# Optimization experiments

Measured on AMD Instinct MI355X. Metric: run time of the kernel, lower is better.

The kernel has to match this reference:

```python
import jax, jax.numpy as jnp
import numpy as np

BATCH = 8192
IN_FEATURES = 4096
OUT_FEATURES = 4096
PACKED_LEN = (IN_FEATURES + 7) // 8  # 512


def _unpack_pm1(x_packed):
    """Unpack uint8-valued ints (stored as int32) into +/-1 float32, LSB-first.
    [.., P] -> [.., P*8]; bit 1 -> +1.0, bit 0 -> -1.0."""
    bits = (x_packed[..., None] >> jnp.arange(8, dtype=x_packed.dtype)) & 1
    bits = bits.reshape(*x_packed.shape[:-1], x_packed.shape[-1] * 8)
    return (2.0 * bits - 1.0).astype(jnp.float32)


def setup_inputs() -> dict:
    key = jax.random.key(0)
    k1, k2, k3 = jax.random.split(key, 3)
    input_packed = jax.random.randint(k1, (BATCH, PACKED_LEN), 0, 256, dtype=jnp.int32)
    weight_packed = jax.random.randint(k2, (OUT_FEATURES, PACKED_LEN), 0, 256, dtype=jnp.int32)
    bias = jax.random.normal(k3, (OUT_FEATURES,), dtype=jnp.float32) * 0.01
    return {"input_packed": input_packed, "weight_packed": weight_packed, "bias": bias}


def reference(input_packed, weight_packed, bias):
    # BitLinear: +/-1 dot product == in_features - 2*popcount(a XOR w)
    a = _unpack_pm1(input_packed)   # [B, in_features]
    w = _unpack_pm1(weight_packed)  # [out_features, in_features]
    out = jnp.einsum('bk,ok->bo', a, w)  # fp32 accumulate, [B, out_features]
    return out + bias
```

## Files before the change

kernel.cpp:

```cpp
#include <hip/hip_runtime.h>
#include <stdint.h>


typedef int v4i  __attribute__((ext_vector_type(4)));
typedef int v16i __attribute__((ext_vector_type(16)));

#define BATCH 8192
#define OUTF  4096
#define KDIM  4096
#define BM    256
#define BN    256
#define BKB   128
#define NSTEP (KDIM / BKB)

__device__ __forceinline__ void expand_word(uint32_t x, uint32_t& pl, uint32_t& ph) {
    uint32_t lo = ((x & 0xFu) * 0x204081u) & 0x01010101u;
    uint32_t hi = (((x >> 4) & 0xFu) * 0x204081u) & 0x01010101u;
    pl = ~((lo << 8) - (lo << 1));
    ph = ~((hi << 8) - (hi << 1));
}

__global__ __launch_bounds__(256) void unpack_kernel(const int* __restrict__ a_packed,
                                                     const int* __restrict__ w_packed,
                                                     char* __restrict__ Ai8,
                                                     char* __restrict__ Wi8) {
    const int A_WORK = BATCH * 32;
    int t = blockIdx.x * 256 + threadIdx.x;
    const int* __restrict__ src = a_packed;
    int4* dst = (int4*)Ai8;
    if (t >= A_WORK) { t -= A_WORK; src = w_packed; dst = (int4*)Wi8; }

    const int r = t & 31;
    const int c = (t >> 5) & 31;
    const int g = t >> 10;
    const int m = g * 32 + r;

    const int4* s4 = (const int4*)src + (m * 128 + c * 4);
    int4 v0 = s4[0], v1 = s4[1], v2 = s4[2], v3 = s4[3];

    int4* dbase = dst + ((g * 32 + c) * 256 + r);

#define EMIT(S, V)                                                     \
    {                                                                  \
        uint32_t l0, h0, l1, h1, l2, h2, l3, h3;                       \
        expand_word((uint32_t)(V).x, l0, h0);                          \
        expand_word((uint32_t)(V).y, l1, h1);                          \
        expand_word((uint32_t)(V).z, l2, h2);                          \
        expand_word((uint32_t)(V).w, l3, h3);                          \
        int4 o0 = make_int4((int)l0, (int)h0, (int)l1, (int)h1);       \
        int4 o1 = make_int4((int)l2, (int)h2, (int)l3, (int)h3);       \
        dbase[(S) * 64]      = o0;                         \
        dbase[(S) * 64 + 32] = o1;                         \
    }
    EMIT(0, v0) EMIT(1, v1) EMIT(2, v2) EMIT(3, v3)
#undef EMIT
}

__global__ __launch_bounds__(512, 2) void bitgemm_mfma(const char* __restrict__ A,
                                                       const char* __restrict__ W,
                                                       const float* __restrict__ bias,
                                                       float* __restrict__ out) {
    __shared__ __attribute__((aligned(16))) char lds[2 * 65536];

    const int tid  = threadIdx.x;
    const int lane = tid & 63;
    const int w    = __builtin_amdgcn_readfirstlane(tid >> 6);
    const int wr   = w >> 2;
    const int wc   = w & 3;
    const int bx   = blockIdx.x;
    const int by   = blockIdx.y;

    const char* baseA = A + (size_t)by * 8 * 131072 + (size_t)lane * 16;
    const char* baseW = W + (size_t)bx * 8 * 131072 + (size_t)lane * 16;

    v16i acc[4][2];
#pragma unroll
    for (int mt = 0; mt < 4; ++mt)
#pragma unroll
        for (int nt = 0; nt < 2; ++nt)
#pragma unroll
            for (int rg = 0; rg < 16; ++rg) acc[mt][nt][rg] = 0;

    auto stage = [&](int kc, int buf) {
        char* ldst = lds + buf * 65536;
#pragma unroll
        for (int j = 0; j < 8; ++j) {
            const int bi = w * 8 + j;
            const char* g;
            if (bi < 32) {
                g = baseA + (bi >> 2) * 131072 + (bi & 3) * 1024 + kc * 4096;
            } else {
                const int b2 = bi - 32;
                g = baseW + (b2 >> 2) * 131072 + (b2 & 3) * 1024 + kc * 4096;
            }
            __builtin_amdgcn_global_load_lds(
                (const __attribute__((address_space(1))) void*)g,
                (__attribute__((address_space(3))) void*)(ldst + bi * 1024),
                16, 0, 0);
        }
    };

    const int aoff = wr * 16384 + lane * 16;
    const int woff = 32768 + wc * 8192 + lane * 16;

    stage(0, 0);
    int cur = 0;
#pragma unroll 1
    for (int kc = 0; kc < NSTEP; ++kc) {
        __syncthreads();
        if (kc < NSTEP - 1) stage(kc + 1, cur ^ 1);

        const char* ldsC = lds + cur * 65536;
#pragma unroll
        for (int s = 0; s < 4; ++s) {
            v4i av[4], wv[2];
#pragma unroll
            for (int mt = 0; mt < 4; ++mt)
                av[mt] = *(const v4i*)(ldsC + aoff + (mt * 4 + s) * 1024);
#pragma unroll
            for (int nt = 0; nt < 2; ++nt)
                wv[nt] = *(const v4i*)(ldsC + woff + (nt * 4 + s) * 1024);
            __builtin_amdgcn_s_setprio(1);
#pragma unroll
            for (int mt = 0; mt < 4; ++mt)
#pragma unroll
                for (int nt = 0; nt < 2; ++nt)
                    acc[mt][nt] = __builtin_amdgcn_mfma_i32_32x32x32_i8(
                        av[mt], wv[nt], acc[mt][nt], 0, 0, 0);
            __builtin_amdgcn_s_setprio(0);
        }
        cur ^= 1;
    }

    const int cl = lane & 31;
    const int r0 = (lane >> 5) * 4;
    const int m0 = by * BM;
    const int n0 = bx * BN;
#pragma unroll
    for (int mt = 0; mt < 4; ++mt) {
        const int rowbase = m0 + (wr * 4 + mt) * 32 + r0;
#pragma unroll
        for (int nt = 0; nt < 2; ++nt) {
            const int col = n0 + (wc * 2 + nt) * 32 + cl;
            const float bv = bias[col];
#pragma unroll
            for (int rg = 0; rg < 16; ++rg) {
                const int row = rowbase + (rg & 3) + 8 * (rg >> 2);
                out[(size_t)row * OUTF + col] = (float)acc[mt][nt][rg] + bv;
            }
        }
    }
}

extern "C" void kernel_launch(void* const* d_in, const int* in_sizes, int n_in,
                              void* d_out, int out_size, void* d_ws, size_t ws_size,
                              hipStream_t stream) {
    const int*   a_packed = (const int*)d_in[0];
    const int*   w_packed = (const int*)d_in[1];
    const float* bias     = (const float*)d_in[2];
    float*       out      = (float*)d_out;

    char* Ai8 = (char*)d_ws;
    char* Wi8 = Ai8 + (size_t)BATCH * KDIM;

    const int total = (BATCH + OUTF) * 32;
    unpack_kernel<<<total / 256, 256, 0, stream>>>(a_packed, w_packed, Ai8, Wi8);

    dim3 grid(OUTF / BN, BATCH / BM);
    bitgemm_mfma<<<grid, 512, 0, stream>>>(Ai8, Wi8, bias, out);
}
```

Before: 259.6 us.

## Deepen GEMM K-loop to a four-buffer pipeline with explicit vmcnt waits

Halves the K chunk per stage and splits the same LDS into four buffers, prefetching three stages ahead instead of one. Each iteration waits only for the oldest stage's global_load_lds via s_waitcnt vmcnt(8), then a raw s_barrier, instead of a full __syncthreads drain. The goal is to keep more global loads in flight while MFMAs run and to hide memory latency. In exchange there are twice as many barriers per K, less MFMA work between them, and hand-counted wait values that must match the number of loads per stage.

```diff
diff --git a/kernel.cpp b/kernel.cpp
--- a/kernel.cpp
+++ b/kernel.cpp
@@ -10,8 +10,12 @@
 #define KDIM  4096
 #define BM    256
 #define BN    256
-#define BKB   128
+#define BKB   64
 #define NSTEP (KDIM / BKB)
+
+#define WAITV8() asm volatile("s_waitcnt vmcnt(8)" ::: "memory")
+#define WAITV4() asm volatile("s_waitcnt vmcnt(4)" ::: "memory")
+#define WAITV0() asm volatile("s_waitcnt vmcnt(0)" ::: "memory")
 
 __device__ __forceinline__ void expand_word(uint32_t x, uint32_t& pl, uint32_t& ph) {
     uint32_t lo = ((x & 0xFu) * 0x204081u) & 0x01010101u;
@@ -60,7 +64,7 @@
                                                        const char* __restrict__ W,
                                                        const float* __restrict__ bias,
                                                        float* __restrict__ out) {
-    __shared__ __attribute__((aligned(16))) char lds[2 * 65536];
+    __shared__ __attribute__((aligned(16))) char lds[4 * 32768];
 
     const int tid  = threadIdx.x;
     const int lane = tid & 63;
@@ -82,16 +86,16 @@
             for (int rg = 0; rg < 16; ++rg) acc[mt][nt][rg] = 0;
 
     auto stage = [&](int kc, int buf) {
-        char* ldst = lds + buf * 65536;
+        char* ldst = lds + buf * 32768;
 #pragma unroll
-        for (int j = 0; j < 8; ++j) {
-            const int bi = w * 8 + j;
+        for (int j = 0; j < 4; ++j) {
+            const int bi = w * 4 + j;
             const char* g;
-            if (bi < 32) {
-                g = baseA + (bi >> 2) * 131072 + (bi & 3) * 1024 + kc * 4096;
+            if (bi < 16) {
+                g = baseA + (bi >> 1) * 131072 + (kc * 2 + (bi & 1)) * 1024;
             } else {
-                const int b2 = bi - 32;
-                g = baseW + (b2 >> 2) * 131072 + (b2 & 3) * 1024 + kc * 4096;
+                const int b2 = bi - 16;
+                g = baseW + (b2 >> 1) * 131072 + (kc * 2 + (b2 & 1)) * 1024;
             }
             __builtin_amdgcn_global_load_lds(
                 (const __attribute__((address_space(1))) void*)g,
@@ -100,26 +104,20 @@
         }
     };
 
-    const int aoff = wr * 16384 + lane * 16;
-    const int woff = 32768 + wc * 8192 + lane * 16;
+    const int aoff = wr * 8192 + lane * 16;
+    const int woff = 16384 + wc * 4096 + lane * 16;
 
-    stage(0, 0);
-    int cur = 0;
-#pragma unroll 1
-    for (int kc = 0; kc < NSTEP; ++kc) {
-        __syncthreads();
-        if (kc < NSTEP - 1) stage(kc + 1, cur ^ 1);
-
-        const char* ldsC = lds + cur * 65536;
+    auto compute = [&](int buf) {
+        const char* ldsC = lds + buf * 32768;
 #pragma unroll
-        for (int s = 0; s < 4; ++s) {
+        for (int sl = 0; sl < 2; ++sl) {
             v4i av[4], wv[2];
 #pragma unroll
             for (int mt = 0; mt < 4; ++mt)
-                av[mt] = *(const v4i*)(ldsC + aoff + (mt * 4 + s) * 1024);
+                av[mt] = *(const v4i*)(ldsC + aoff + (mt * 2 + sl) * 1024);
 #pragma unroll
             for (int nt = 0; nt < 2; ++nt)
-                wv[nt] = *(const v4i*)(ldsC + woff + (nt * 4 + s) * 1024);
+                wv[nt] = *(const v4i*)(ldsC + woff + (nt * 2 + sl) * 1024);
             __builtin_amdgcn_s_setprio(1);
 #pragma unroll
             for (int mt = 0; mt < 4; ++mt)
@@ -129,8 +127,25 @@
                         av[mt], wv[nt], acc[mt][nt], 0, 0, 0);
             __builtin_amdgcn_s_setprio(0);
         }
-        cur ^= 1;
+    };
+
+    stage(0, 0);
+    stage(1, 1);
+    stage(2, 2);
+
+#pragma unroll 1
+    for (int kc = 0; kc < NSTEP - 2; ++kc) {
+        WAITV8();
+        __builtin_amdgcn_s_barrier();
+        if (kc < NSTEP - 3) stage(kc + 3, (kc + 3) & 3);
+        compute(kc & 3);
     }
+    WAITV4();
+    __builtin_amdgcn_s_barrier();
+    compute((NSTEP - 2) & 3);
+    WAITV0();
+    __builtin_amdgcn_s_barrier();
+    compute((NSTEP - 1) & 3);
 
     const int cl = lane & 31;
     const int r0 = (lane >> 5) * 4;
```

Result: slower. 267.2 us (+2.9%).

## Load A fragments directly to registers and stage only W through LDS

Applied to the files above, without the earlier changes.

A-operand fragments now go straight from global memory into registers, double-buffered across two register sets, and only W tiles are staged into LDS via global_load_lds. The K step is halved and LDS shrinks from 128KB to 32KB. The aim is to cut LDS traffic and capacity pressure so more blocks fit per CU. In exchange, A is loaded redundantly by the four wave columns that share a row group, and register pressure from two A buffers rises.

```diff
diff --git a/kernel.cpp b/kernel.cpp
--- a/kernel.cpp
+++ b/kernel.cpp
@@ -10,7 +10,7 @@
 #define KDIM  4096
 #define BM    256
 #define BN    256
-#define BKB   128
+#define BKB   64
 #define NSTEP (KDIM / BKB)
 
 __device__ __forceinline__ void expand_word(uint32_t x, uint32_t& pl, uint32_t& ph) {
@@ -60,7 +60,7 @@
                                                        const char* __restrict__ W,
                                                        const float* __restrict__ bias,
                                                        float* __restrict__ out) {
-    __shared__ __attribute__((aligned(16))) char lds[2 * 65536];
+    __shared__ __attribute__((aligned(16))) char lds[2 * 16384];
 
     const int tid  = threadIdx.x;
     const int lane = tid & 63;
@@ -70,8 +70,8 @@
     const int bx   = blockIdx.x;
     const int by   = blockIdx.y;
 
-    const char* baseA = A + (size_t)by * 8 * 131072 + (size_t)lane * 16;
-    const char* baseW = W + (size_t)bx * 8 * 131072 + (size_t)lane * 16;
+    const char* pAw = A + (size_t)(by * 8 + wr * 4) * 131072 + (size_t)lane * 16;
+    const char* pWs = W + (size_t)(bx * 8 + w) * 131072 + (size_t)lane * 16;
 
     v16i acc[4][2];
 #pragma unroll
@@ -81,55 +81,55 @@
 #pragma unroll
             for (int rg = 0; rg < 16; ++rg) acc[mt][nt][rg] = 0;
 
-    auto stage = [&](int kc, int buf) {
-        char* ldst = lds + buf * 65536;
+    auto loadA = [&](v4i (&dst)[4][2], int kc) {
 #pragma unroll
-        for (int j = 0; j < 8; ++j) {
-            const int bi = w * 8 + j;
-            const char* g;
-            if (bi < 32) {
-                g = baseA + (bi >> 2) * 131072 + (bi & 3) * 1024 + kc * 4096;
-            } else {
-                const int b2 = bi - 32;
-                g = baseW + (b2 >> 2) * 131072 + (b2 & 3) * 1024 + kc * 4096;
+        for (int mt = 0; mt < 4; ++mt)
+#pragma unroll
+            for (int sl = 0; sl < 2; ++sl)
+                dst[mt][sl] = *(const v4i*)(pAw + mt * 131072 + (kc * 2 + sl) * 1024);
+    };
+
+    auto stageW = [&](int kc, int buf) {
+        char* ldst = lds + buf * 16384 + w * 2048;
+#pragma unroll
+        for (int sl = 0; sl < 2; ++sl)
+            __builtin_amdgcn_global_load_lds(
+                (const __attribute__((address_space(1))) void*)(pWs + (kc * 2 + sl) * 1024),
+                (__attribute__((address_space(3))) void*)(ldst + sl * 1024),
+                16, 0, 0);
+    };
+
+    auto compute = [&](const v4i (&av)[4][2], int buf) {
+        const char* ldsC = lds + buf * 16384 + wc * 4096 + lane * 16;
+#pragma unroll
+        for (int sl = 0; sl < 2; ++sl) {
+            v4i wv0 = *(const v4i*)(ldsC + sl * 1024);
+            v4i wv1 = *(const v4i*)(ldsC + 2048 + sl * 1024);
+            __builtin_amdgcn_s_setprio(1);
+#pragma unroll
+            for (int mt = 0; mt < 4; ++mt) {
+                acc[mt][0] = __builtin_amdgcn_mfma_i32_32x32x32_i8(av[mt][sl], wv0,
+                                                                   acc[mt][0], 0, 0, 0);
+                acc[mt][1] = __builtin_amdgcn_mfma_i32_32x32x32_i8(av[mt][sl], wv1,
+                                                                   acc[mt][1], 0, 0, 0);
             }
-            __builtin_amdgcn_global_load_lds(
-                (const __attribute__((address_space(1))) void*)g,
-                (__attribute__((address_space(3))) void*)(ldst + bi * 1024),
-                16, 0, 0);
+            __builtin_amdgcn_s_setprio(0);
         }
     };
 
-    const int aoff = wr * 16384 + lane * 16;
-    const int woff = 32768 + wc * 8192 + lane * 16;
+    v4i aA[4][2], aB[4][2];
 
-    stage(0, 0);
-    int cur = 0;
+    loadA(aA, 0);
+    stageW(0, 0);
+
 #pragma unroll 1
-    for (int kc = 0; kc < NSTEP; ++kc) {
+    for (int kc = 0; kc < NSTEP; kc += 2) {
         __syncthreads();
-        if (kc < NSTEP - 1) stage(kc + 1, cur ^ 1);
-
-        const char* ldsC = lds + cur * 65536;
-#pragma unroll
-        for (int s = 0; s < 4; ++s) {
-            v4i av[4], wv[2];
-#pragma unroll
-            for (int mt = 0; mt < 4; ++mt)
-                av[mt] = *(const v4i*)(ldsC + aoff + (mt * 4 + s) * 1024);
-#pragma unroll
-            for (int nt = 0; nt < 2; ++nt)
-                wv[nt] = *(const v4i*)(ldsC + woff + (nt * 4 + s) * 1024);
-            __builtin_amdgcn_s_setprio(1);
-#pragma unroll
-            for (int mt = 0; mt < 4; ++mt)
-#pragma unroll
-                for (int nt = 0; nt < 2; ++nt)
-                    acc[mt][nt] = __builtin_amdgcn_mfma_i32_32x32x32_i8(
-                        av[mt], wv[nt], acc[mt][nt], 0, 0, 0);
-            __builtin_amdgcn_s_setprio(0);
-        }
-        cur ^= 1;
+        if (kc + 1 < NSTEP) { loadA(aB, kc + 1); stageW(kc + 1, 1); }
+        compute(aA, 0);
+        __syncthreads();
+        if (kc + 2 < NSTEP) { loadA(aA, kc + 2); stageW(kc + 2, 0); }
+        compute(aB, 1);
     }
 
     const int cl = lane & 31;
```

Measured after the change: 280.5 us. 8.0% more time.

## Keep operands bit-packed and expand to 0/1 int8 in registers before MFMA

Applied to the files above, without the earlier changes.

The prepass now only repacks the int32-stored bytes into a dense 1-bit layout (512 B per row) instead of writing an expanded ±1 int8 matrix. The GEMM loads the packed bits straight from global memory into registers, without LDS, and expands them to 0/1 bytes for the int8 MFMA. It recovers the ±1 dot product algebraically from per-row popcounts: 4*acc - 2*popA - 2*popW + K. This cuts workspace traffic and removes LDS staging and barriers, at the cost of more VALU expansion work per MFMA and uncoalesced per-thread 16-byte global loads.

```diff
diff --git a/kernel.cpp b/kernel.cpp
--- a/kernel.cpp
+++ b/kernel.cpp
@@ -10,68 +10,65 @@
 #define KDIM  4096
 #define BM    256
 #define BN    256
-#define BKB   128
-#define NSTEP (KDIM / BKB)
+#define NPAIR 32
 
-__device__ __forceinline__ void expand_word(uint32_t x, uint32_t& pl, uint32_t& ph) {
-    uint32_t lo = ((x & 0xFu) * 0x204081u) & 0x01010101u;
-    uint32_t hi = (((x >> 4) & 0xFu) * 0x204081u) & 0x01010101u;
-    pl = ~((lo << 8) - (lo << 1));
-    ph = ~((hi << 8) - (hi << 1));
+__device__ __forceinline__ uint32_t pack4(int4 q) {
+    return (uint32_t)q.x | ((uint32_t)q.y << 8) |
+           ((uint32_t)q.z << 16) | ((uint32_t)q.w << 24);
 }
 
-__global__ __launch_bounds__(256) void unpack_kernel(const int* __restrict__ a_packed,
-                                                     const int* __restrict__ w_packed,
-                                                     char* __restrict__ Ai8,
-                                                     char* __restrict__ Wi8) {
-    const int A_WORK = BATCH * 32;
+__global__ __launch_bounds__(256) void bitpack(const int* __restrict__ ap,
+                                               const int* __restrict__ wp,
+                                               uint4* __restrict__ Ab,
+                                               uint4* __restrict__ Wb) {
     int t = blockIdx.x * 256 + threadIdx.x;
-    const int* __restrict__ src = a_packed;
-    int4* dst = (int4*)Ai8;
-    if (t >= A_WORK) { t -= A_WORK; src = w_packed; dst = (int4*)Wi8; }
-
-    const int r = t & 31;
-    const int c = (t >> 5) & 31;
-    const int g = t >> 10;
-    const int m = g * 32 + r;
-
-    const int4* s4 = (const int4*)src + (m * 128 + c * 4);
-    int4 v0 = s4[0], v1 = s4[1], v2 = s4[2], v3 = s4[3];
-
-    int4* dbase = dst + ((g * 32 + c) * 256 + r);
-
-#define EMIT(S, V)                                                     \
-    {                                                                  \
-        uint32_t l0, h0, l1, h1, l2, h2, l3, h3;                       \
-        expand_word((uint32_t)(V).x, l0, h0);                          \
-        expand_word((uint32_t)(V).y, l1, h1);                          \
-        expand_word((uint32_t)(V).z, l2, h2);                          \
-        expand_word((uint32_t)(V).w, l3, h3);                          \
-        int4 o0 = make_int4((int)l0, (int)h0, (int)l1, (int)h1);       \
-        int4 o1 = make_int4((int)l2, (int)h2, (int)l3, (int)h3);       \
-        dbase[(S) * 64]      = o0;                         \
-        dbase[(S) * 64 + 32] = o1;                         \
+    const int* src;
+    uint4* dst;
+    if (t < BATCH * NPAIR) {
+        const int p = t >> 13, m = t & 8191;
+        src = ap + m * 512 + p * 16;
+        dst = Ab + (p * BATCH + m);
+    } else {
+        const int u = t - BATCH * NPAIR;
+        const int p = u >> 12, n = u & 4095;
+        src = wp + n * 512 + p * 16;
+        dst = Wb + (p * OUTF + n);
     }
-    EMIT(0, v0) EMIT(1, v1) EMIT(2, v2) EMIT(3, v3)
-#undef EMIT
+    const int4* s4 = (const int4*)src;
+    int4 q0 = s4[0], q1 = s4[1], q2 = s4[2], q3 = s4[3];
+    uint4 o;
+    o.x = pack4(q0); o.y = pack4(q1); o.z = pack4(q2); o.w = pack4(q3);
+    *dst = o;
 }
 
-__global__ __launch_bounds__(512, 2) void bitgemm_mfma(const char* __restrict__ A,
-                                                       const char* __restrict__ W,
-                                                       const float* __restrict__ bias,
-                                                       float* __restrict__ out) {
-    __shared__ __attribute__((aligned(16))) char lds[2 * 65536];
+__device__ __forceinline__ uint32_t spread4(uint32_t n) {
+    return (n * 0x204081u) & 0x01010101u;
+}
+__device__ __forceinline__ v4i expand16(uint32_t x) {
+    v4i r;
+    r[0] = (int)spread4(x & 0xFu);
+    r[1] = (int)spread4((x >> 4) & 0xFu);
+    r[2] = (int)spread4((x >> 8) & 0xFu);
+    r[3] = (int)spread4(x >> 12);
+    return r;
+}
 
+__global__ __launch_bounds__(512, 2) void bitgemm_fused(const v4i* __restrict__ Ab,
+                                                        const v4i* __restrict__ Wb,
+                                                        const float* __restrict__ bias,
+                                                        float* __restrict__ out) {
     const int tid  = threadIdx.x;
     const int lane = tid & 63;
     const int w    = __builtin_amdgcn_readfirstlane(tid >> 6);
     const int wr   = w >> 2;
     const int wc   = w & 3;
+    const int rl   = lane & 31;
+    const int hl16 = (lane >> 5) * 16;
     const int bx   = blockIdx.x;
     const int by   = blockIdx.y;
 
-    const char* baseA = A + (size_t)by * 8 * 131072 + (size_t)lane * 16;
-    const char* baseW = W + (size_t)bx * 8 * 131072 + (size_t)lane * 16;
+    const int rowA0 = by * 256 + wr * 128 + rl;
+    const int rowW0 = bx * 256 + wc * 64 + rl;
 
     v16i acc[4][2];
 #pragma unroll
@@ -81,55 +78,56 @@
 #pragma unroll
             for (int rg = 0; rg < 16; ++rg) acc[mt][nt][rg] = 0;
 
-    auto stage = [&](int kc, int buf) {
-        char* ldst = lds + buf * 65536;
+    int ars[4] = {0, 0, 0, 0};
+    int wrs[2] = {0, 0};
+
+    auto loadPair = [&](v4i (&pa)[4], v4i (&pw)[2], int p) {
 #pragma unroll
-        for (int j = 0; j < 8; ++j) {
-            const int bi = w * 8 + j;
-            const char* g;
-            if (bi < 32) {
-                g = baseA + (bi >> 2) * 131072 + (bi & 3) * 1024 + kc * 4096;
-            } else {
-                const int b2 = bi - 32;
-                g = baseW + (b2 >> 2) * 131072 + (b2 & 3) * 1024 + kc * 4096;
+        for (int mt = 0; mt < 4; ++mt)
+            pa[mt] = Ab[(size_t)p * BATCH + rowA0 + mt * 32];
+#pragma unroll
+        for (int nt = 0; nt < 2; ++nt)
+            pw[nt] = Wb[(size_t)p * OUTF + rowW0 + nt * 32];
+    };
+
+    auto computePair = [&](const v4i (&pa)[4], const v4i (&pw)[2]) {
+#pragma unroll
+        for (int mt = 0; mt < 4; ++mt)
+            ars[mt] += __popc((uint32_t)pa[mt][0]) + __popc((uint32_t)pa[mt][1]) +
+                       __popc((uint32_t)pa[mt][2]) + __popc((uint32_t)pa[mt][3]);
+#pragma unroll
+        for (int nt = 0; nt < 2; ++nt)
+            wrs[nt] += __popc((uint32_t)pw[nt][0]) + __popc((uint32_t)pw[nt][1]) +
+                       __popc((uint32_t)pw[nt][2]) + __popc((uint32_t)pw[nt][3]);
+#pragma unroll
+        for (int c = 0; c < 4; ++c) {
+            v4i av[4], wv[2];
+#pragma unroll
+            for (int mt = 0; mt < 4; ++mt)
+                av[mt] = expand16(((uint32_t)pa[mt][c] >> hl16) & 0xFFFFu);
+#pragma unroll
+            for (int nt = 0; nt < 2; ++nt)
+                wv[nt] = expand16(((uint32_t)pw[nt][c] >> hl16) & 0xFFFFu);
+            __builtin_amdgcn_s_setprio(1);
+#pragma unroll
+            for (int mt = 0; mt < 4; ++mt) {
+                acc[mt][0] = __builtin_amdgcn_mfma_i32_32x32x32_i8(av[mt], wv[0],
+                                                                   acc[mt][0], 0, 0, 0);
+                acc[mt][1] = __builtin_amdgcn_mfma_i32_32x32x32_i8(av[mt], wv[1],
+                                                                   acc[mt][1], 0, 0, 0);
             }
-            __builtin_amdgcn_global_load_lds(
-                (const __attribute__((address_space(1))) void*)g,
-                (__attribute__((address_space(3))) void*)(ldst + bi * 1024),
-                16, 0, 0);
+            __builtin_amdgcn_s_setprio(0);
         }
     };
 
-    const int aoff = wr * 16384 + lane * 16;
-    const int woff = 32768 + wc * 8192 + lane * 16;
-
-    stage(0, 0);
-    int cur = 0;
+    v4i pa0[4], pw0[2], pa1[4], pw1[2];
+    loadPair(pa0, pw0, 0);
 #pragma unroll 1
-    for (int kc = 0; kc < NSTEP; ++kc) {
-        __syncthreads();
-        if (kc < NSTEP - 1) stage(kc + 1, cur ^ 1);
-
-        const char* ldsC = lds + cur * 65536;
-#pragma unroll
-        for (int s = 0; s < 4; ++s) {
-            v4i av[4], wv[2];
-#pragma unroll
-            for (int mt = 0; mt < 4; ++mt)
-                av[mt] = *(const v4i*)(ldsC + aoff + (mt * 4 + s) * 1024);
-#pragma unroll
-            for (int nt = 0; nt < 2; ++nt)
-                wv[nt] = *(const v4i*)(ldsC + woff + (nt * 4 + s) * 1024);
-            __builtin_amdgcn_s_setprio(1);
-#pragma unroll
-            for (int mt = 0; mt < 4; ++mt)
-#pragma unroll
-                for (int nt = 0; nt < 2; ++nt)
-                    acc[mt][nt] = __builtin_amdgcn_mfma_i32_32x32x32_i8(
-                        av[mt], wv[nt], acc[mt][nt], 0, 0, 0);
-            __builtin_amdgcn_s_setprio(0);
-        }
-        cur ^= 1;
+    for (int pp = 0; pp < NPAIR / 2; ++pp) {
+        loadPair(pa1, pw1, 2 * pp + 1);
+        computePair(pa0, pw0);
+        if (pp < NPAIR / 2 - 1) loadPair(pa0, pw0, 2 * pp + 2);
+        computePair(pa1, pw1);
     }
 
     const int cl = lane & 31;
@@ -138,15 +136,18 @@
     const int n0 = bx * BN;
 #pragma unroll
     for (int mt = 0; mt < 4; ++mt) {
-        const int rowbase = m0 + (wr * 4 + mt) * 32 + r0;
 #pragma unroll
         for (int nt = 0; nt < 2; ++nt) {
             const int col = n0 + (wc * 2 + nt) * 32 + cl;
             const float bv = bias[col];
+            const int rw2 = 2 * wrs[nt];
 #pragma unroll
             for (int rg = 0; rg < 16; ++rg) {
-                const int row = rowbase + (rg & 3) + 8 * (rg >> 2);
-                out[(size_t)row * OUTF + col] = (float)acc[mt][nt][rg] + bv;
+                const int rig = r0 + (rg & 3) + 8 * (rg >> 2);
+                const int ra  = __shfl(ars[mt], rig);
+                const int v   = 4 * acc[mt][nt][rg] - 2 * ra - rw2 + KDIM;
+                const int row = m0 + (wr * 4 + mt) * 32 + rig;
+                out[(size_t)row * OUTF + col] = (float)v + bv;
             }
         }
     }
@@ -160,12 +161,13 @@
     const float* bias     = (const float*)d_in[2];
     float*       out      = (float*)d_out;
 
-    char* Ai8 = (char*)d_ws;
-    char* Wi8 = Ai8 + (size_t)BATCH * KDIM;
+    uint4* Ab = (uint4*)d_ws;
+    uint4* Wb = (uint4*)((char*)d_ws + (size_t)BATCH * 512);
 
-    const int total = (BATCH + OUTF) * 32;
-    unpack_kernel<<<total / 256, 256, 0, stream>>>(a_packed, w_packed, Ai8, Wi8);
+    const int total = (BATCH + OUTF) * NPAIR;
+    bitpack<<<total / 256, 256, 0, stream>>>(a_packed, w_packed, Ab, Wb);
 
     dim3 grid(OUTF / BN, BATCH / BM);
-    bitgemm_mfma<<<grid, 512, 0, stream>>>(Ai8, Wi8, bias, out);
+    bitgemm_fused<<<grid, 512, 0, stream>>>((const v4i*)Ab, (const v4i*)Wb,
+                                            bias, out);
 }
```

New measurement: 259.2 us. No clear change (-0.2%).
